# Performance work log

Hardware: AMD Instinct MI355X
Metric: run time of the kernel (lower is better)

## Reference

```python
import jax, jax.numpy as jnp
import numpy as np

B, C, H, T, K = 8, 512, 512, 4096, 2


def _conv1d_causal(x, w, b):
    # x: [B, C, T], w: [H, C, K] (torch Conv1d layout OIH), causal left-pad K-1 zeros
    k = w.shape[-1]
    y = jax.lax.conv_general_dilated(
        x, w, window_strides=(1,), padding=[(k - 1, 0)],
        dimension_numbers=("NCH", "OIH", "NCH"))
    return y + b[None, :, None]


def setup_inputs() -> dict:
    key = jax.random.key(0)
    ks = jax.random.split(key, 5)
    scale = 1.0 / np.sqrt(C * K)  # torch Conv1d default init scale
    inp = {"x": jax.random.normal(ks[0], (B, C, T), dtype=jnp.float32)}
    for name, k in zip("zfoi", ks[1:]):
        inp["w" + name] = jax.random.uniform(k, (H, C, K), jnp.float32, -scale, scale)
        inp["b" + name] = jnp.zeros((H,), jnp.float32)
    return inp


def reference(x, wz, bz, wf, bf, wo, bo, wi, bi):
    # QRNN 'ifo' pooling: c_t = f_t * c_{t-1} + i_t * z_t;  h_t = o_t * c_t
    z = jnp.tanh(_conv1d_causal(x, wz, bz))
    f = jax.nn.sigmoid(_conv1d_causal(x, wf, bf))  # zoneout p=0 -> identity
    o = jax.nn.sigmoid(_conv1d_causal(x, wo, bo))
    i = jax.nn.sigmoid(_conv1d_causal(x, wi, bi))
    g = i * z  # [B, H, T]

    fT = jnp.moveaxis(f, 2, 0)  # [T, B, H]
    gT = jnp.moveaxis(g, 2, 0)

    def step(c, fg):
        ft, gt = fg
        c = ft * c + gt
        return c, c

    c0 = jnp.zeros((x.shape[0], wz.shape[0]), dtype=x.dtype)
    _, cT = jax.lax.scan(step, c0, (fT, gT))
    c = jnp.moveaxis(cT, 0, 2)  # [B, H, T]
    return o * c
```

## Files before the change

### kernel.cpp

```cpp
#include <hip/hip_runtime.h>
#include <hip/hip_bf16.h>
#include <cstdint>

typedef _Float16 half8 __attribute__((ext_vector_type(8)));
typedef float f32x4 __attribute__((ext_vector_type(4)));

#define B_DIM 8
#define C_DIM 512
#define H_DIM 512
#define T_DIM 4096
#define KTOT 1024
#define MTOT 2048

__device__ __forceinline__ void gload16(const void* g, void* l) {
  __builtin_amdgcn_global_load_lds(
      (const __attribute__((address_space(1))) unsigned int*)g,
      (__attribute__((address_space(3))) unsigned int*)l, 16, 0, 0);
}

__device__ __forceinline__ float sigmoidf_(float x) { return 1.0f / (1.0f + expf(-x)); }

__global__ __launch_bounds__(256) void pack_w(
    const float* __restrict__ wz, const float* __restrict__ wf,
    const float* __restrict__ wo, const float* __restrict__ wi,
    _Float16* __restrict__ A16) {
  int idx = blockIdx.x * 256 + threadIdx.x;
  int m = idx >> 10, k = idx & 1023;
  int h = m >> 2, g = m & 3;
  int j = k >> 9, c = k & 511;
  const float* w = (g == 0) ? wz : (g == 1) ? wf : (g == 2) ? wo : wi;
  A16[idx] = (_Float16)w[(h << 10) + (c << 1) + j];
}

__global__ __launch_bounds__(256) void transpose_x(
    const float* __restrict__ x, _Float16* __restrict__ XT) {
  int bid = blockIdx.x;
  int b = bid >> 9;
  int rem = bid & 511;
  int c0 = (rem >> 6) * 64;
  int t0 = (rem & 63) * 64;
  __shared__ _Float16 tile[64][73];
  int tid = threadIdx.x;
#pragma unroll
  for (int it = 0; it < 4; ++it) {
    int idx = it * 256 + tid;
    int ci = idx >> 4, tc = idx & 15;
    float4 v = *(const float4*)(x + (((size_t)b * C_DIM + c0 + ci) * T_DIM + t0 + tc * 4));
    tile[ci][tc * 4 + 0] = (_Float16)v.x;
    tile[ci][tc * 4 + 1] = (_Float16)v.y;
    tile[ci][tc * 4 + 2] = (_Float16)v.z;
    tile[ci][tc * 4 + 3] = (_Float16)v.w;
  }
  __syncthreads();
#pragma unroll
  for (int it = 0; it < 2; ++it) {
    int idx = it * 256 + tid;
    int tr = idx >> 3, cb = idx & 7;
    half8 h;
#pragma unroll
    for (int e = 0; e < 8; ++e) h[e] = tile[cb * 8 + e][tr];
    int t = t0 + tr;
    size_t rowbase = ((size_t)b * T_DIM + t) * KTOT;
    *(half8*)(XT + rowbase + 512 + c0 + cb * 8) = h;
    if (t + 1 < T_DIM)
      *(half8*)(XT + rowbase + KTOT + c0 + cb * 8) = h;
  }
  if (t0 == 0 && tid < 8) {
    half8 z = {};
    *(half8*)(XT + ((size_t)b * T_DIM) * KTOT + c0 + tid * 8) = z;
  }
}

__global__ __launch_bounds__(256, 2) void qrnn_gemm(
    const _Float16* __restrict__ A16, const _Float16* __restrict__ XT,
    const float* __restrict__ bz, const float* __restrict__ bf,
    const float* __restrict__ bo, const float* __restrict__ bi,
    _Float16* __restrict__ F, _Float16* __restrict__ G, _Float16* __restrict__ O) {
  __shared__ _Float16 lA[128 * 64];
  __shared__ _Float16 lB[128 * 64];
  int bid = blockIdx.x;
  int b = bid >> 9;
  int rem = bid & 511;
  int m0 = (rem >> 5) * 128;
  int t0 = (rem & 31) * 128;
  int tid = threadIdx.x;
  int lane = tid & 63, wid = tid >> 6;
  int wm = (wid >> 1) * 64, wn = (wid & 1) * 64;

  f32x4 acc[4][4];
#pragma unroll
  for (int i = 0; i < 4; ++i)
#pragma unroll
    for (int j = 0; j < 4; ++j) acc[i][j] = (f32x4){0.f, 0.f, 0.f, 0.f};

  const _Float16* Ab = A16 + (size_t)m0 * KTOT;
  const _Float16* Bb = XT + ((size_t)b * T_DIM + t0) * KTOT;

  for (int kt = 0; kt < 16; ++kt) {
    int k0 = kt * 64;
#pragma unroll
    for (int it = 0; it < 4; ++it) {
      int idx = it * 256 + tid;
      int row = idx >> 3, blk = idx & 7;
      int gblk = blk ^ (row & 7);
      gload16(Ab + (size_t)row * KTOT + k0 + gblk * 8, (char*)lA + idx * 16);
    }
#pragma unroll
    for (int it = 0; it < 4; ++it) {
      int idx = it * 256 + tid;
      int row = idx >> 3, blk = idx & 7;
      int gblk = blk ^ (row & 7);
      gload16(Bb + (size_t)row * KTOT + k0 + gblk * 8, (char*)lB + idx * 16);
    }
    __syncthreads();
#pragma unroll
    for (int ks = 0; ks < 2; ++ks) {
      half8 av[4], bv[4];
#pragma unroll
      for (int i = 0; i < 4; ++i) {
        int row = wm + i * 16 + (lane & 15);
        int blk = (ks * 4 + (lane >> 4)) ^ (row & 7);
        av[i] = *(const half8*)(lA + row * 64 + blk * 8);
      }
#pragma unroll
      for (int j = 0; j < 4; ++j) {
        int row = wn + j * 16 + (lane & 15);
        int blk = (ks * 4 + (lane >> 4)) ^ (row & 7);
        bv[j] = *(const half8*)(lB + row * 64 + blk * 8);
      }
#pragma unroll
      for (int i = 0; i < 4; ++i)
#pragma unroll
        for (int j = 0; j < 4; ++j)
          acc[i][j] = __builtin_amdgcn_mfma_f32_16x16x32_f16(av[i], bv[j], acc[i][j], 0, 0, 0);
    }
    __syncthreads();
  }

#pragma unroll
  for (int i = 0; i < 4; ++i) {
    int h = ((m0 + wm + i * 16) >> 2) + (lane >> 4);
    float vbz = bz[h], vbf = bf[h], vbo = bo[h], vbi = bi[h];
#pragma unroll
    for (int j = 0; j < 4; ++j) {
      int t = t0 + wn + j * 16 + (lane & 15);
      float yz = acc[i][j][0] + vbz;
      float yf = acc[i][j][1] + vbf;
      float yo = acc[i][j][2] + vbo;
      float yi = acc[i][j][3] + vbi;
      float zz = tanhf(yz);
      float ff = sigmoidf_(yf);
      float oo = sigmoidf_(yo);
      float ii = sigmoidf_(yi);
      size_t gi = ((size_t)b * H_DIM + h) * T_DIM + t;
      F[gi] = (_Float16)ff;
      G[gi] = (_Float16)(ii * zz);
      O[gi] = (_Float16)oo;
    }
  }
}

__global__ __launch_bounds__(256) void scan_fused(
    const _Float16* __restrict__ F, const _Float16* __restrict__ G,
    const _Float16* __restrict__ O, float* __restrict__ out) {
  __shared__ char smem[24 * 1024 + 64];
  _Float16* sF = (_Float16*)smem;
  _Float16* sG = (_Float16*)(smem + 8192);
  _Float16* sO = (_Float16*)(smem + 16384);
  float* sOut = (float*)smem;
  float* wFs = (float*)(smem + 24576);
  float* wGs = wFs + 4;

  int tid = threadIdx.x;
  int lane = tid & 63, wv = tid >> 6;
  size_t base = (size_t)blockIdx.x * T_DIM;
  const _Float16* Fg = F + base;
  const _Float16* Gg = G + base;
  const _Float16* Og = O + base;

#pragma unroll
  for (int it = 0; it < 2; ++it) {
    int idx = it * 256 + tid;
    int sb = idx ^ ((idx >> 3) & 7);
    gload16(Fg + sb * 8, (char*)sF + idx * 16);
    gload16(Gg + sb * 8, (char*)sG + idx * 16);
    gload16(Og + sb * 8, (char*)sO + idx * 16);
  }
  asm volatile("s_waitcnt vmcnt(0)");
  __syncthreads();

  int i = tid;
  int b0 = (2 * i) ^ (((2 * i) >> 3) & 7);
  int b1 = (2 * i + 1) ^ (((2 * i + 1) >> 3) & 7);
  half8 f0 = *(half8*)((char*)sF + b0 * 16);
  half8 f1 = *(half8*)((char*)sF + b1 * 16);
  half8 g0 = *(half8*)((char*)sG + b0 * 16);
  half8 g1 = *(half8*)((char*)sG + b1 * 16);
  half8 o0 = *(half8*)((char*)sO + b0 * 16);
  half8 o1 = *(half8*)((char*)sO + b1 * 16);

  float Fp = 1.f, Gc = 0.f;
#pragma unroll
  for (int e = 0; e < 8; ++e) {
    float fe = (float)f0[e];
    Gc = fe * Gc + (float)g0[e];
    Fp *= fe;
  }
#pragma unroll
  for (int e = 0; e < 8; ++e) {
    float fe = (float)f1[e];
    Gc = fe * Gc + (float)g1[e];
    Fp *= fe;
  }

  float Fs = Fp, Gs = Gc;
#pragma unroll
  for (int d = 1; d < 64; d <<= 1) {
    float Fo = __shfl_up(Fs, d);
    float Go = __shfl_up(Gs, d);
    if (lane >= d) { Gs = Fs * Go + Gs; Fs = Fs * Fo; }
  }
  if (lane == 63) { wFs[wv] = Fs; wGs[wv] = Gs; }
  __syncthreads();
  float carry = 0.f;
  for (int w = 0; w < wv; ++w) carry = wFs[w] * carry + wGs[w];
  float Fpr = __shfl_up(Fs, 1);
  float Gpr = __shfl_up(Gs, 1);
  float cin = (lane == 0) ? carry : Fpr * carry + Gpr;

  float c = cin;
  float4 r0, r1, r2, r3;
#define QSTEP(fv, gv, ov, e, dst) \
  { c = (float)fv[e] * c + (float)gv[e]; dst = (float)ov[e] * c; }
  QSTEP(f0, g0, o0, 0, r0.x) QSTEP(f0, g0, o0, 1, r0.y)
  QSTEP(f0, g0, o0, 2, r0.z) QSTEP(f0, g0, o0, 3, r0.w)
  QSTEP(f0, g0, o0, 4, r1.x) QSTEP(f0, g0, o0, 5, r1.y)
  QSTEP(f0, g0, o0, 6, r1.z) QSTEP(f0, g0, o0, 7, r1.w)
  QSTEP(f1, g1, o1, 0, r2.x) QSTEP(f1, g1, o1, 1, r2.y)
  QSTEP(f1, g1, o1, 2, r2.z) QSTEP(f1, g1, o1, 3, r2.w)
  QSTEP(f1, g1, o1, 4, r3.x) QSTEP(f1, g1, o1, 5, r3.y)
  QSTEP(f1, g1, o1, 6, r3.z) QSTEP(f1, g1, o1, 7, r3.w)
#undef QSTEP
  {
    int obl = 4 * i;
    int s0 = (obl + 0) ^ (((obl + 0) >> 3) & 7);
    int s1 = (obl + 1) ^ (((obl + 1) >> 3) & 7);
    int s2 = (obl + 2) ^ (((obl + 2) >> 3) & 7);
    int s3 = (obl + 3) ^ (((obl + 3) >> 3) & 7);
    *(float4*)((char*)sOut + s0 * 16) = r0;
    *(float4*)((char*)sOut + s1 * 16) = r1;
    *(float4*)((char*)sOut + s2 * 16) = r2;
    *(float4*)((char*)sOut + s3 * 16) = r3;
  }
  __syncthreads();

  float* og = out + base;
#pragma unroll
  for (int it = 0; it < 4; ++it) {
    int idx = it * 256 + tid;
    int sb = idx ^ ((idx >> 3) & 7);
    *(float4*)(og + idx * 4) = *(float4*)((char*)sOut + sb * 16);
  }
}

extern "C" void kernel_launch(void* const* d_in, const int* in_sizes, int n_in,
                              void* d_out, int out_size, void* d_ws, size_t ws_size,
                              hipStream_t stream) {
  (void)in_sizes; (void)n_in; (void)out_size; (void)ws_size;
  const float* x  = (const float*)d_in[0];
  const float* wz = (const float*)d_in[1];
  const float* bz = (const float*)d_in[2];
  const float* wf = (const float*)d_in[3];
  const float* bf = (const float*)d_in[4];
  const float* wo = (const float*)d_in[5];
  const float* bo = (const float*)d_in[6];
  const float* wi = (const float*)d_in[7];
  const float* bi = (const float*)d_in[8];

  char* ws = (char*)d_ws;
  const size_t MB = 1ull << 20;
  _Float16* A16 = (_Float16*)(ws);
  _Float16* XT  = (_Float16*)(ws + 4 * MB);
  _Float16* F   = (_Float16*)(ws + 68 * MB);
  _Float16* G   = (_Float16*)(ws + 100 * MB);
  _Float16* O   = (_Float16*)(ws + 132 * MB);

  pack_w<<<(MTOT * KTOT) / 256, 256, 0, stream>>>(wz, wf, wo, wi, A16);
  transpose_x<<<B_DIM * 8 * 64, 256, 0, stream>>>(x, XT);
  qrnn_gemm<<<B_DIM * 16 * 32, 256, 0, stream>>>(A16, XT, bz, bf, bo, bi, F, G, O);
  scan_fused<<<B_DIM * H_DIM, 256, 0, stream>>>(F, G, O, (float*)d_out);
}
```

Before: 320.3 us.

## Rewrite GEMM as 256x256 tiled, double-buffered pipeline with compact shifted X layout

The fused conv GEMM moves from 128x128 tiles with a synchronous load-then-compute loop to 256x256 tiles on 512 threads. It uses a double-buffered 128KB dynamic-LDS pipeline with four phases per K-step, interleaving async global-to-LDS loads with MFMA and raising wave priority during compute. The transposed X buffer no longer stores both time-shifted copies. It keeps a single padded [T+1]x512 layout and reads the previous timestep via a negative offset, which halves transpose writes and the workspace. Block IDs are swizzled for cache locality. The large LDS footprint limits the kernel to one block per CU, and the hand-counted vmcnt waits are fragile.

```diff
diff --git a/kernel.cpp b/kernel.cpp
--- a/kernel.cpp
+++ b/kernel.cpp
@@ -33,7 +33,7 @@
 }
 
 __global__ __launch_bounds__(256) void transpose_x(
-    const float* __restrict__ x, _Float16* __restrict__ XT) {
+    const float* __restrict__ x, _Float16* __restrict__ XTg) {
   int bid = blockIdx.x;
   int b = bid >> 9;
   int rem = bid & 511;
@@ -60,90 +60,168 @@
 #pragma unroll
     for (int e = 0; e < 8; ++e) h[e] = tile[cb * 8 + e][tr];
     int t = t0 + tr;
-    size_t rowbase = ((size_t)b * T_DIM + t) * KTOT;
-    *(half8*)(XT + rowbase + 512 + c0 + cb * 8) = h;
-    if (t + 1 < T_DIM)
-      *(half8*)(XT + rowbase + KTOT + c0 + cb * 8) = h;
+    *(half8*)(XTg + ((size_t)b * (T_DIM + 1) + 1 + t) * 512 + c0 + cb * 8) = h;
   }
   if (t0 == 0 && tid < 8) {
     half8 z = {};
-    *(half8*)(XT + ((size_t)b * T_DIM) * KTOT + c0 + tid * 8) = z;
-  }
-}
-
-__global__ __launch_bounds__(256, 2) void qrnn_gemm(
-    const _Float16* __restrict__ A16, const _Float16* __restrict__ XT,
+    *(half8*)(XTg + ((size_t)b * (T_DIM + 1)) * 512 + c0 + tid * 8) = z;
+  }
+}
+
+__global__ __launch_bounds__(512, 2) void qrnn_gemm2(
+    const _Float16* __restrict__ A16, const _Float16* __restrict__ XTg,
     const float* __restrict__ bz, const float* __restrict__ bf,
     const float* __restrict__ bo, const float* __restrict__ bi,
     _Float16* __restrict__ F, _Float16* __restrict__ G, _Float16* __restrict__ O) {
-  __shared__ _Float16 lA[128 * 64];
-  __shared__ _Float16 lB[128 * 64];
+  extern __shared__ char lds[];
   int bid = blockIdx.x;
-  int b = bid >> 9;
-  int rem = bid & 511;
-  int m0 = (rem >> 5) * 128;
-  int t0 = (rem & 31) * 128;
+  int swz = (bid & 7) * 128 + (bid >> 3);
+  int b = swz >> 7;
+  int rem = swz & 127;
+  int t0 = (rem >> 3) * 256;
+  int m0 = (rem & 7) * 256;
   int tid = threadIdx.x;
   int lane = tid & 63, wid = tid >> 6;
-  int wm = (wid >> 1) * 64, wn = (wid & 1) * 64;
-
-  f32x4 acc[4][4];
-#pragma unroll
-  for (int i = 0; i < 4; ++i)
+  int wr = wid >> 2, wc = wid & 3;
+  int lg = lane >> 4, l7 = lane & 7, l15 = lane & 15;
+
+  int blkoff0 = (lg ^ l7) << 4;
+  int blkoff1 = ((4 + lg) ^ l7) << 4;
+  int aoffA[4], boffB[4];
+#pragma unroll
+  for (int ii = 0; ii < 4; ++ii) aoffA[ii] = (wr * 64 + ii * 16 + l15) * 128;
+#pragma unroll
+  for (int nf = 0; nf < 4; ++nf)
+    boffB[nf] = 32768 + (nf >> 1) * 16384 + (wc * 32 + (nf & 1) * 16 + l15) * 128;
+
+  int srow = tid >> 3;
+  int gblk = (tid & 7) ^ (srow & 7);
+  int aStageOff = (m0 + srow) * 1024 + gblk * 8;
+  size_t bStageOff =
+      ((size_t)b * (T_DIM + 1) + 1 + t0 + (srow >> 5) * 64 + (srow & 31)) * 512 + gblk * 8;
+
+  auto stageA = [&](int q, int u2) {
+    char* dst = lds + ((u2 & 1) << 16) + q * 16384 + tid * 16;
+    const _Float16* g = A16 + aStageOff + q * 65536 + u2 * 64;
+    gload16(g, dst);
+    gload16(g + 131072, dst + 8192);
+  };
+  auto stageB = [&](int s, int u2) {
+    char* dst = lds + ((u2 & 1) << 16) + 32768 + s * 16384 + tid * 16;
+    const _Float16* g = XTg + bStageOff + s * 16384 + ((u2 & 7) << 6)
+                        - ((u2 < 8) ? 512 : 0);
+    gload16(g, dst);
+    gload16(g + 65536, dst + 8192);
+  };
+
+  f32x4 acc[8][4];
+#pragma unroll
+  for (int i = 0; i < 8; ++i)
 #pragma unroll
     for (int j = 0; j < 4; ++j) acc[i][j] = (f32x4){0.f, 0.f, 0.f, 0.f};
-
-  const _Float16* Ab = A16 + (size_t)m0 * KTOT;
-  const _Float16* Bb = XT + ((size_t)b * T_DIM + t0) * KTOT;
-
-  for (int kt = 0; kt < 16; ++kt) {
-    int k0 = kt * 64;
-#pragma unroll
-    for (int it = 0; it < 4; ++it) {
-      int idx = it * 256 + tid;
-      int row = idx >> 3, blk = idx & 7;
-      int gblk = blk ^ (row & 7);
-      gload16(Ab + (size_t)row * KTOT + k0 + gblk * 8, (char*)lA + idx * 16);
-    }
-#pragma unroll
-    for (int it = 0; it < 4; ++it) {
-      int idx = it * 256 + tid;
-      int row = idx >> 3, blk = idx & 7;
-      int gblk = blk ^ (row & 7);
-      gload16(Bb + (size_t)row * KTOT + k0 + gblk * 8, (char*)lB + idx * 16);
-    }
-    __syncthreads();
-#pragma unroll
-    for (int ks = 0; ks < 2; ++ks) {
-      half8 av[4], bv[4];
-#pragma unroll
-      for (int i = 0; i < 4; ++i) {
-        int row = wm + i * 16 + (lane & 15);
-        int blk = (ks * 4 + (lane >> 4)) ^ (row & 7);
-        av[i] = *(const half8*)(lA + row * 64 + blk * 8);
+  half8 a[4][2], bb[4][2];
+
+  stageA(0, 0); stageB(0, 0); stageB(1, 0); stageA(1, 0);
+  stageA(0, 1); stageB(0, 1); stageB(1, 1); stageA(1, 1);
+  asm volatile("s_waitcnt vmcnt(8)" ::: "memory");
+  __builtin_amdgcn_sched_barrier(0);
+  __builtin_amdgcn_s_barrier();
+  __builtin_amdgcn_sched_barrier(0);
+
+#define PHASE_TAIL()                                         \
+  __builtin_amdgcn_sched_barrier(0);                         \
+  __builtin_amdgcn_s_barrier();                              \
+  asm volatile("s_waitcnt lgkmcnt(0)" ::: "memory");         \
+  __builtin_amdgcn_sched_barrier(0);                         \
+  __builtin_amdgcn_s_setprio(1);
+
+#define PHASE_END()                                          \
+  __builtin_amdgcn_s_setprio(0);                             \
+  __builtin_amdgcn_sched_barrier(0);                         \
+  __builtin_amdgcn_s_barrier();                              \
+  __builtin_amdgcn_sched_barrier(0);
+
+  for (int u = 0; u < 16; ++u) {
+    int dbuf = (u & 1) << 16;
+#pragma unroll
+    for (int ii = 0; ii < 4; ++ii) {
+      a[ii][0] = *(const half8*)(lds + dbuf + aoffA[ii] + blkoff0);
+      a[ii][1] = *(const half8*)(lds + dbuf + aoffA[ii] + blkoff1);
+    }
+#pragma unroll
+    for (int nf = 0; nf < 2; ++nf) {
+      bb[nf][0] = *(const half8*)(lds + dbuf + boffB[nf] + blkoff0);
+      bb[nf][1] = *(const half8*)(lds + dbuf + boffB[nf] + blkoff1);
+    }
+    if (u >= 1 && u <= 14) stageB(1, u + 1);
+    PHASE_TAIL()
+#pragma unroll
+    for (int ii = 0; ii < 4; ++ii)
+#pragma unroll
+      for (int nf = 0; nf < 2; ++nf) {
+        acc[ii][nf] = __builtin_amdgcn_mfma_f32_16x16x32_f16(a[ii][0], bb[nf][0], acc[ii][nf], 0, 0, 0);
+        acc[ii][nf] = __builtin_amdgcn_mfma_f32_16x16x32_f16(a[ii][1], bb[nf][1], acc[ii][nf], 0, 0, 0);
       }
-#pragma unroll
-      for (int j = 0; j < 4; ++j) {
-        int row = wn + j * 16 + (lane & 15);
-        int blk = (ks * 4 + (lane >> 4)) ^ (row & 7);
-        bv[j] = *(const half8*)(lB + row * 64 + blk * 8);
+    PHASE_END()
+
+#pragma unroll
+    for (int nf = 2; nf < 4; ++nf) {
+      bb[nf][0] = *(const half8*)(lds + dbuf + boffB[nf] + blkoff0);
+      bb[nf][1] = *(const half8*)(lds + dbuf + boffB[nf] + blkoff1);
+    }
+    if (u <= 13) stageA(0, u + 2);
+    PHASE_TAIL()
+#pragma unroll
+    for (int ii = 0; ii < 4; ++ii)
+#pragma unroll
+      for (int nf = 2; nf < 4; ++nf) {
+        acc[ii][nf] = __builtin_amdgcn_mfma_f32_16x16x32_f16(a[ii][0], bb[nf][0], acc[ii][nf], 0, 0, 0);
+        acc[ii][nf] = __builtin_amdgcn_mfma_f32_16x16x32_f16(a[ii][1], bb[nf][1], acc[ii][nf], 0, 0, 0);
       }
-#pragma unroll
-      for (int i = 0; i < 4; ++i)
-#pragma unroll
-        for (int j = 0; j < 4; ++j)
-          acc[i][j] = __builtin_amdgcn_mfma_f32_16x16x32_f16(av[i], bv[j], acc[i][j], 0, 0, 0);
-    }
-    __syncthreads();
-  }
-
-#pragma unroll
-  for (int i = 0; i < 4; ++i) {
-    int h = ((m0 + wm + i * 16) >> 2) + (lane >> 4);
+    PHASE_END()
+
+#pragma unroll
+    for (int ii = 0; ii < 4; ++ii) {
+      a[ii][0] = *(const half8*)(lds + dbuf + 16384 + aoffA[ii] + blkoff0);
+      a[ii][1] = *(const half8*)(lds + dbuf + 16384 + aoffA[ii] + blkoff1);
+    }
+    if (u <= 13) stageB(0, u + 2);
+    PHASE_TAIL()
+#pragma unroll
+    for (int ii = 0; ii < 4; ++ii)
+#pragma unroll
+      for (int nf = 0; nf < 2; ++nf) {
+        acc[4 + ii][nf] = __builtin_amdgcn_mfma_f32_16x16x32_f16(a[ii][0], bb[nf][0], acc[4 + ii][nf], 0, 0, 0);
+        acc[4 + ii][nf] = __builtin_amdgcn_mfma_f32_16x16x32_f16(a[ii][1], bb[nf][1], acc[4 + ii][nf], 0, 0, 0);
+      }
+    PHASE_END()
+
+    if (u <= 13) stageA(1, u + 2);
+    if (u < 14) {
+      asm volatile("s_waitcnt vmcnt(6)" ::: "memory");
+    } else if (u == 14) {
+      asm volatile("s_waitcnt vmcnt(0)" ::: "memory");
+    }
+    PHASE_TAIL()
+#pragma unroll
+    for (int ii = 0; ii < 4; ++ii)
+#pragma unroll
+      for (int nf = 2; nf < 4; ++nf) {
+        acc[4 + ii][nf] = __builtin_amdgcn_mfma_f32_16x16x32_f16(a[ii][0], bb[nf][0], acc[4 + ii][nf], 0, 0, 0);
+        acc[4 + ii][nf] = __builtin_amdgcn_mfma_f32_16x16x32_f16(a[ii][1], bb[nf][1], acc[4 + ii][nf], 0, 0, 0);
+      }
+    PHASE_END()
+  }
+#undef PHASE_TAIL
+#undef PHASE_END
+
+#pragma unroll
+  for (int i = 0; i < 8; ++i) {
+    int h = ((m0 + wr * 128 + i * 16) >> 2) + lg;
     float vbz = bz[h], vbf = bf[h], vbo = bo[h], vbi = bi[h];
 #pragma unroll
     for (int j = 0; j < 4; ++j) {
-      int t = t0 + wn + j * 16 + (lane & 15);
+      int t = t0 + wc * 64 + j * 16 + l15;
       float yz = acc[i][j][0] + vbz;
       float yf = acc[i][j][1] + vbf;
       float yo = acc[i][j][2] + vbo;
@@ -151,10 +229,10 @@
       float zz = tanhf(yz);
       float ff = sigmoidf_(yf);
       float oo = sigmoidf_(yo);
-      float ii = sigmoidf_(yi);
+      float ii2 = sigmoidf_(yi);
       size_t gi = ((size_t)b * H_DIM + h) * T_DIM + t;
       F[gi] = (_Float16)ff;
-      G[gi] = (_Float16)(ii * zz);
+      G[gi] = (_Float16)(ii2 * zz);
       O[gi] = (_Float16)oo;
     }
   }
@@ -186,7 +264,7 @@
     gload16(Gg + sb * 8, (char*)sG + idx * 16);
     gload16(Og + sb * 8, (char*)sO + idx * 16);
   }
-  asm volatile("s_waitcnt vmcnt(0)");
+  asm volatile("s_waitcnt vmcnt(0)" ::: "memory");
   __syncthreads();
 
   int i = tid;
@@ -280,13 +358,16 @@
   char* ws = (char*)d_ws;
   const size_t MB = 1ull << 20;
   _Float16* A16 = (_Float16*)(ws);
-  _Float16* XT  = (_Float16*)(ws + 4 * MB);
-  _Float16* F   = (_Float16*)(ws + 68 * MB);
-  _Float16* G   = (_Float16*)(ws + 100 * MB);
-  _Float16* O   = (_Float16*)(ws + 132 * MB);
+  _Float16* XTg = (_Float16*)(ws + 4 * MB);
+  _Float16* F   = (_Float16*)(ws + 40 * MB);
+  _Float16* G   = (_Float16*)(ws + 72 * MB);
+  _Float16* O   = (_Float16*)(ws + 104 * MB);
+
+  hipFuncSetAttribute((const void*)qrnn_gemm2,
+                      hipFuncAttributeMaxDynamicSharedMemorySize, 131072);
 
   pack_w<<<(MTOT * KTOT) / 256, 256, 0, stream>>>(wz, wf, wo, wi, A16);
-  transpose_x<<<B_DIM * 8 * 64, 256, 0, stream>>>(x, XT);
-  qrnn_gemm<<<B_DIM * 16 * 32, 256, 0, stream>>>(A16, XT, bz, bf, bo, bi, F, G, O);
+  transpose_x<<<B_DIM * 8 * 64, 256, 0, stream>>>(x, XTg);
+  qrnn_gemm2<<<B_DIM * 8 * 16, 512, 131072, stream>>>(A16, XTg, bz, bf, bo, bi, F, G, O);
   scan_fused<<<B_DIM * H_DIM, 256, 0, stream>>>(F, G, O, (float*)d_out);
 }
```

Result: slower. 329.5 us (+2.9%).

## Store X once with shifted-row reads and fuse prep kernels into one launch

Applied to the files above, without the earlier changes.

The duplicated im2col layout of X (two copies per row for the two conv taps) becomes a single transposed fp16 buffer with one zero pad row per batch. The GEMM reads the previous time step for tap 0 by shifting the row pointer. The weight pack and X transpose are merged into one launch, and the weight pack now uses float2 loads. The GEMM also raises its occupancy hint to 4 blocks per CU and remaps block IDs to interleave batches. The aim is to halve the XT write traffic and workspace and to drop a launch, at the cost of possible register pressure from the tighter launch bound.

```diff
diff --git a/kernel.cpp b/kernel.cpp
--- a/kernel.cpp
+++ b/kernel.cpp
@@ -20,67 +20,66 @@
 
 __device__ __forceinline__ float sigmoidf_(float x) { return 1.0f / (1.0f + expf(-x)); }
 
-__global__ __launch_bounds__(256) void pack_w(
+__global__ __launch_bounds__(256) void prep(
+    const float* __restrict__ x,
     const float* __restrict__ wz, const float* __restrict__ wf,
     const float* __restrict__ wo, const float* __restrict__ wi,
-    _Float16* __restrict__ A16) {
-  int idx = blockIdx.x * 256 + threadIdx.x;
-  int m = idx >> 10, k = idx & 1023;
-  int h = m >> 2, g = m & 3;
-  int j = k >> 9, c = k & 511;
-  const float* w = (g == 0) ? wz : (g == 1) ? wf : (g == 2) ? wo : wi;
-  A16[idx] = (_Float16)w[(h << 10) + (c << 1) + j];
-}
-
-__global__ __launch_bounds__(256) void transpose_x(
-    const float* __restrict__ x, _Float16* __restrict__ XT) {
+    _Float16* __restrict__ XTg, _Float16* __restrict__ A16) {
+  __shared__ _Float16 tile[64][73];
   int bid = blockIdx.x;
-  int b = bid >> 9;
-  int rem = bid & 511;
-  int c0 = (rem >> 6) * 64;
-  int t0 = (rem & 63) * 64;
-  __shared__ _Float16 tile[64][73];
   int tid = threadIdx.x;
-#pragma unroll
-  for (int it = 0; it < 4; ++it) {
-    int idx = it * 256 + tid;
-    int ci = idx >> 4, tc = idx & 15;
-    float4 v = *(const float4*)(x + (((size_t)b * C_DIM + c0 + ci) * T_DIM + t0 + tc * 4));
-    tile[ci][tc * 4 + 0] = (_Float16)v.x;
-    tile[ci][tc * 4 + 1] = (_Float16)v.y;
-    tile[ci][tc * 4 + 2] = (_Float16)v.z;
-    tile[ci][tc * 4 + 3] = (_Float16)v.w;
-  }
-  __syncthreads();
-#pragma unroll
-  for (int it = 0; it < 2; ++it) {
-    int idx = it * 256 + tid;
-    int tr = idx >> 3, cb = idx & 7;
-    half8 h;
-#pragma unroll
-    for (int e = 0; e < 8; ++e) h[e] = tile[cb * 8 + e][tr];
-    int t = t0 + tr;
-    size_t rowbase = ((size_t)b * T_DIM + t) * KTOT;
-    *(half8*)(XT + rowbase + 512 + c0 + cb * 8) = h;
-    if (t + 1 < T_DIM)
-      *(half8*)(XT + rowbase + KTOT + c0 + cb * 8) = h;
-  }
-  if (t0 == 0 && tid < 8) {
-    half8 z = {};
-    *(half8*)(XT + ((size_t)b * T_DIM) * KTOT + c0 + tid * 8) = z;
-  }
-}
-
-__global__ __launch_bounds__(256, 2) void qrnn_gemm(
-    const _Float16* __restrict__ A16, const _Float16* __restrict__ XT,
+  if (bid < 4096) {
+    int b = bid >> 9;
+    int rem = bid & 511;
+    int c0 = (rem >> 6) * 64;
+    int t0 = (rem & 63) * 64;
+#pragma unroll
+    for (int it = 0; it < 4; ++it) {
+      int idx = it * 256 + tid;
+      int ci = idx >> 4, tc = idx & 15;
+      float4 v = *(const float4*)(x + (((size_t)b * C_DIM + c0 + ci) * T_DIM + t0 + tc * 4));
+      tile[ci][tc * 4 + 0] = (_Float16)v.x;
+      tile[ci][tc * 4 + 1] = (_Float16)v.y;
+      tile[ci][tc * 4 + 2] = (_Float16)v.z;
+      tile[ci][tc * 4 + 3] = (_Float16)v.w;
+    }
+    __syncthreads();
+#pragma unroll
+    for (int it = 0; it < 2; ++it) {
+      int idx = it * 256 + tid;
+      int tr = idx >> 3, cb = idx & 7;
+      half8 h;
+#pragma unroll
+      for (int e = 0; e < 8; ++e) h[e] = tile[cb * 8 + e][tr];
+      int t = t0 + tr;
+      *(half8*)(XTg + ((size_t)b * (T_DIM + 1) + 1 + t) * 512 + c0 + cb * 8) = h;
+    }
+    if (t0 == 0 && tid < 8) {
+      half8 z = {};
+      *(half8*)(XTg + ((size_t)b * (T_DIM + 1)) * 512 + c0 + tid * 8) = z;
+    }
+  } else {
+    int idx = (bid - 4096) * 256 + tid;
+    int m = idx >> 9, c = idx & 511;
+    int h = m >> 2, g = m & 3;
+    const float* w = (g == 0) ? wz : (g == 1) ? wf : (g == 2) ? wo : wi;
+    float2 v = *(const float2*)(w + (h << 10) + (c << 1));
+    A16[(size_t)m * KTOT + c] = (_Float16)v.x;
+    A16[(size_t)m * KTOT + 512 + c] = (_Float16)v.y;
+  }
+}
+
+__global__ __launch_bounds__(256, 4) void qrnn_gemm(
+    const _Float16* __restrict__ A16, const _Float16* __restrict__ XTg,
     const float* __restrict__ bz, const float* __restrict__ bf,
     const float* __restrict__ bo, const float* __restrict__ bi,
     _Float16* __restrict__ F, _Float16* __restrict__ G, _Float16* __restrict__ O) {
   __shared__ _Float16 lA[128 * 64];
   __shared__ _Float16 lB[128 * 64];
   int bid = blockIdx.x;
-  int b = bid >> 9;
-  int rem = bid & 511;
+  int gbid = (bid & 7) * 512 + (bid >> 3);
+  int b = gbid >> 9;
+  int rem = gbid & 511;
   int m0 = (rem >> 5) * 128;
   int t0 = (rem & 31) * 128;
   int tid = threadIdx.x;
@@ -94,10 +93,12 @@
     for (int j = 0; j < 4; ++j) acc[i][j] = (f32x4){0.f, 0.f, 0.f, 0.f};
 
   const _Float16* Ab = A16 + (size_t)m0 * KTOT;
-  const _Float16* Bb = XT + ((size_t)b * T_DIM + t0) * KTOT;
+  const _Float16* Bb = XTg + ((size_t)b * (T_DIM + 1) + 1 + t0) * 512;
 
   for (int kt = 0; kt < 16; ++kt) {
     int k0 = kt * 64;
+    int cp = k0 & 511;
+    int jofs = (k0 < 512) ? 512 : 0;
 #pragma unroll
     for (int it = 0; it < 4; ++it) {
       int idx = it * 256 + tid;
@@ -110,7 +111,7 @@
       int idx = it * 256 + tid;
       int row = idx >> 3, blk = idx & 7;
       int gblk = blk ^ (row & 7);
-      gload16(Bb + (size_t)row * KTOT + k0 + gblk * 8, (char*)lB + idx * 16);
+      gload16(Bb + (size_t)(row * 512) - jofs + cp + gblk * 8, (char*)lB + idx * 16);
     }
     __syncthreads();
 #pragma unroll
@@ -186,7 +187,7 @@
     gload16(Gg + sb * 8, (char*)sG + idx * 16);
     gload16(Og + sb * 8, (char*)sO + idx * 16);
   }
-  asm volatile("s_waitcnt vmcnt(0)");
+  asm volatile("s_waitcnt vmcnt(0)" ::: "memory");
   __syncthreads();
 
   int i = tid;
@@ -280,13 +281,12 @@
   char* ws = (char*)d_ws;
   const size_t MB = 1ull << 20;
   _Float16* A16 = (_Float16*)(ws);
-  _Float16* XT  = (_Float16*)(ws + 4 * MB);
-  _Float16* F   = (_Float16*)(ws + 68 * MB);
-  _Float16* G   = (_Float16*)(ws + 100 * MB);
-  _Float16* O   = (_Float16*)(ws + 132 * MB);
-
-  pack_w<<<(MTOT * KTOT) / 256, 256, 0, stream>>>(wz, wf, wo, wi, A16);
-  transpose_x<<<B_DIM * 8 * 64, 256, 0, stream>>>(x, XT);
-  qrnn_gemm<<<B_DIM * 16 * 32, 256, 0, stream>>>(A16, XT, bz, bf, bo, bi, F, G, O);
+  _Float16* XTg = (_Float16*)(ws + 4 * MB);
+  _Float16* F   = (_Float16*)(ws + 40 * MB);
+  _Float16* G   = (_Float16*)(ws + 72 * MB);
+  _Float16* O   = (_Float16*)(ws + 104 * MB);
+
+  prep<<<4096 + 4096, 256, 0, stream>>>(x, wz, wf, wo, wi, XTg, A16);
+  qrnn_gemm<<<B_DIM * 16 * 32, 256, 0, stream>>>(A16, XTg, bz, bf, bo, bi, F, G, O);
   scan_fused<<<B_DIM * H_DIM, 256, 0, stream>>>(F, G, O, (float*)d_out);
 }
```

Measured after the change: 327.1 us. 1.02x slower.
